# Kernel tuning notes

Measured on AMD Instinct MI355X. Metric: run time of the kernel, lower is better.

Reference implementation:

```python
import jax, jax.numpy as jnp
import numpy as np

C = 128          # num_channels
HID = 256        # mlp hidden = 2*C
HEAD_DIM = 16    # C // num_heads (8)
SCALE = 1.0 / np.sqrt(HEAD_DIM)
EPS = 1e-5


def _linear_init(key, fan_in, fan_out):
    kw, kb = jax.random.split(key)
    s = 1.0 / np.sqrt(fan_in)
    w = jax.random.uniform(kw, (fan_in, fan_out), minval=-s, maxval=s, dtype=jnp.float32)
    b = jax.random.uniform(kb, (fan_out,), minval=-s, maxval=s, dtype=jnp.float32)
    return w, b


def setup_inputs() -> dict:
    key = jax.random.key(0)
    ks = jax.random.split(key, 8)
    x = jax.random.normal(ks[0], (4, C, 64, 64), dtype=jnp.float32)
    wq, bq = _linear_init(ks[1], C, C)
    wk, bk = _linear_init(ks[2], C, C)
    wv, bv = _linear_init(ks[3], C, C)
    wo, bo = _linear_init(ks[4], C, C)
    w1, b1 = _linear_init(ks[5], C, HID)
    w2, b2 = _linear_init(ks[6], HID, C)
    return {
        "x": x,
        "ln1_w": jnp.ones((C,), jnp.float32), "ln1_b": jnp.zeros((C,), jnp.float32),
        "wq": wq, "bq": bq, "wk": wk, "bk": bk, "wv": wv, "bv": bv,
        "wo": wo, "bo": bo,
        "ln2_w": jnp.ones((C,), jnp.float32), "ln2_b": jnp.zeros((C,), jnp.float32),
        "w1": w1, "b1": b1, "w2": w2, "b2": b2,
    }


def _layernorm(x, w, b):
    mu = jnp.mean(x, axis=-1, keepdims=True)
    var = jnp.mean(jnp.square(x - mu), axis=-1, keepdims=True)
    return (x - mu) * jax.lax.rsqrt(var + EPS) * w + b


def reference(x, ln1_w, ln1_b, wq, bq, wk, bk, wv, bv, wo, bo, ln2_w, ln2_b, w1, b1, w2, b2):
    B, Cc, H, W = x.shape
    t = x.reshape(B, Cc, H * W).transpose(0, 2, 1)  # [B, S, C]
    xl = _layernorm(t, ln1_w, ln1_b)
    q = xl @ wq + bq
    k = xl @ wk + bk
    v = xl @ wv + bv
    scores = jnp.einsum('bqc,bkc->bqk', q, k) * SCALE  # [B, S, S]
    # Faithful to source: softmax over dim=1 (the QUERY axis).
    attn = jax.nn.softmax(scores, axis=1)
    att_out = jnp.einsum('bqk,bkc->bqc', attn, v) @ wo + bo
    t = att_out + t
    m = _layernorm(t, ln2_w, ln2_b) @ w1 + b1
    m = jax.nn.gelu(m, approximate=False) @ w2 + b2
    t = jax.nn.gelu(m, approximate=False) + t  # second GELU per source
    return t.transpose(0, 2, 1).reshape(B, Cc, H, W)
```

## Files before the change

kernel.cpp:

```cpp
#include <hip/hip_runtime.h>
#include <math.h>

#define S 4096
#define CNUM 128
#define BATCH 4
#define MTOT (BATCH * S)
#define SCLOG2E 0.36067376022224085f
#define EPSLN 1e-5f
#define KSPLIT 4
#define QSPLIT 8


typedef __attribute__((ext_vector_type(8))) short bf16x8;
typedef __attribute__((ext_vector_type(4))) float f32x4;
typedef __attribute__((ext_vector_type(16))) float f32x16;
typedef __attribute__((ext_vector_type(4))) unsigned int u32x4;

__device__ __forceinline__ float gelu_exact(float x) {
    return 0.5f * x * (1.0f + erff(x * 0.7071067811865476f));
}

__device__ __forceinline__ unsigned short f2b(float f) {
    union { float f; unsigned int u; } v; v.f = f;
    unsigned int r = (v.u + 0x7FFFu + ((v.u >> 16) & 1u)) >> 16;
    return (unsigned short)r;
}
__device__ __forceinline__ float b2f(unsigned short u) {
    return __uint_as_float((unsigned)u << 16);
}
__device__ __forceinline__ int swz(int col, int row) {
    return ((((col >> 3) ^ (row & 15)) << 3) | (col & 7));
}

__device__ __forceinline__ void gl_lds16(const void* g, void* l) {
    __builtin_amdgcn_global_load_lds(
        (__attribute__((address_space(1))) void*)g,
        (__attribute__((address_space(3))) void*)l, 16, 0, 0);
}

__global__ __launch_bounds__(256) void ln1_transpose(
    const float* __restrict__ x, const float* __restrict__ w, const float* __restrict__ bb,
    unsigned short* __restrict__ xlh, float* __restrict__ t)
{
    __shared__ float tile[128][65];
    __shared__ float mu[64], rs[64];
    const int b = blockIdx.y;
    const int s0 = blockIdx.x * 64;
    const float* xb = x + (size_t)b * CNUM * S;
    for (int i = threadIdx.x; i < 128 * 64; i += 256) {
        int c = i >> 6, sl = i & 63;
        tile[c][sl] = xb[(size_t)c * S + s0 + sl];
    }
    __syncthreads();
    if (threadIdx.x < 64) {
        float sum = 0.f, sq = 0.f;
        for (int c = 0; c < 128; ++c) {
            float v = tile[c][threadIdx.x];
            sum += v; sq += v * v;
        }
        float m = sum * (1.f / 128.f);
        float var = sq * (1.f / 128.f) - m * m;
        mu[threadIdx.x] = m;
        rs[threadIdx.x] = rsqrtf(var + EPSLN);
    }
    __syncthreads();
    for (int i = threadIdx.x; i < 128 * 64; i += 256) {
        int c = i & 127, sl = i >> 7;
        float v = tile[c][sl];
        size_t row = (size_t)b * S + s0 + sl;
        t[row * CNUM + c] = v;
        xlh[row * CNUM + swz(c, sl)] = f2b((v - mu[sl]) * rs[sl] * w[c] + bb[c]);
    }
}

__global__ __launch_bounds__(256) void convw(
    const float* __restrict__ wq, const float* __restrict__ wk, const float* __restrict__ wv,
    const float* __restrict__ wo, const float* __restrict__ w1, const float* __restrict__ w2,
    const float* __restrict__ bq, const float* __restrict__ bk, const float* __restrict__ bv,
    unsigned short* __restrict__ wqkvh, unsigned short* __restrict__ woh,
    unsigned short* __restrict__ w1h, unsigned short* __restrict__ w2h,
    float* __restrict__ bqkv)
{
    int a = blockIdx.y;
    int idx = blockIdx.x * 256 + threadIdx.x;
    if (a == 6) {
        if (idx < 128) bqkv[idx] = bq[idx];
        else if (idx < 256) bqkv[idx] = bk[idx - 128];
        else if (idx < 384) bqkv[idx] = bv[idx - 256];
        return;
    }
    const float* src; unsigned short* dst; int Nsh, Ksz;
    switch (a) {
        case 0: src = wq; dst = wqkvh;          Nsh = 7; Ksz = 128; break;
        case 1: src = wk; dst = wqkvh + 16384;  Nsh = 7; Ksz = 128; break;
        case 2: src = wv; dst = wqkvh + 32768;  Nsh = 7; Ksz = 128; break;
        case 3: src = wo; dst = woh;            Nsh = 7; Ksz = 128; break;
        case 4: src = w1; dst = w1h;            Nsh = 8; Ksz = 128; break;
        default: src = w2; dst = w2h;           Nsh = 7; Ksz = 256; break;
    }
    int total = Ksz << Nsh;
    if (idx >= total) return;
    int k = idx >> Nsh, n = idx & ((1 << Nsh) - 1);
    dst[n * Ksz + swz(k, n)] = f2b(src[idx]);
}

template<int KT, int EPI, int BM>
__global__ __launch_bounds__(256) void gemm_mfma(
    const unsigned short* __restrict__ A, const unsigned short* __restrict__ Bt,
    const float* __restrict__ bias, const float* __restrict__ res,
    void* __restrict__ Cv, void* __restrict__ Cv2,
    const float* __restrict__ wln, const float* __restrict__ bln, int N)
{
    constexpr int CH = KT / 8;
    constexpr int CSH = (KT == 128) ? 4 : 5;
    constexpr int BKT = (KT == 256) ? 128 : KT;
    constexpr int NPH = KT / BKT;
    constexpr int NJ = (BM == 64) ? 4 : 2;
    constexpr int NG = 128 / (NJ * 16);
    __shared__ unsigned short As[BM * KT];
    __shared__ unsigned short Bs[128 * BKT];
    __shared__ float2 lnred[(EPI == 3) ? NG * BM : 1];
    const int bm = blockIdx.y * BM;
    const int bn = blockIdx.x * 128;
    const int z = blockIdx.z;
    const unsigned short* Btz = (EPI == 7) ? Bt + z * 16384 : Bt;
    const float* biasz = (EPI == 7) ? bias + z * 128 : bias;
    const int tid = threadIdx.x;
    const int w = tid >> 6, l = tid & 63;
    const int rw = (BM == 64) ? (w & 1) * 32 : 0;
    const int cw = (BM == 64) ? (w >> 1) * 64 : w * 32;
    const int lm = l & 15, lq = l >> 4;

    f32x4 zero = {0.f, 0.f, 0.f, 0.f};
    f32x4 acc[2][NJ];
    #pragma unroll
    for (int i = 0; i < 2; ++i)
        #pragma unroll
        for (int j = 0; j < NJ; ++j) acc[i][j] = zero;

    #pragma unroll
    for (int ph = 0; ph < NPH; ++ph) {
        if (ph == 0) {
            if (EPI == 3) {
                #pragma unroll
                for (int i = 0; i < (BM * CH) / 256; ++i) {
                    int cid = i * 256 + tid;
                    int r = cid >> CSH, c = cid & (CH - 1);
                    int p = (c & ~15) | ((c ^ r) & 15);
                    float s8[8];
                    #pragma unroll
                    for (int j = 0; j < 8; ++j) s8[j] = 0.f;
                    #pragma unroll
                    for (int pp = 0; pp < KSPLIT; ++pp) {
                        const unsigned short* src = A + (size_t)pp * ((size_t)MTOT * CNUM)
                                                      + (size_t)(bm + r) * KT + c * 8;
                        ushort4 u0 = *(const ushort4*)(src);
                        ushort4 u1 = *(const ushort4*)(src + 4);
                        s8[0] += b2f(u0.x); s8[1] += b2f(u0.y); s8[2] += b2f(u0.z); s8[3] += b2f(u0.w);
                        s8[4] += b2f(u1.x); s8[5] += b2f(u1.y); s8[6] += b2f(u1.z); s8[7] += b2f(u1.w);
                    }
                    ushort4 o0, o1;
                    o0.x = f2b(s8[0]); o0.y = f2b(s8[1]); o0.z = f2b(s8[2]); o0.w = f2b(s8[3]);
                    o1.x = f2b(s8[4]); o1.y = f2b(s8[5]); o1.z = f2b(s8[6]); o1.w = f2b(s8[7]);
                    *(ushort4*)(As + r * KT + p * 8) = o0;
                    *(ushort4*)(As + r * KT + p * 8 + 4) = o1;
                }
            } else {
                #pragma unroll
                for (int i = 0; i < (BM * CH) / 256; ++i)
                    gl_lds16(A + (size_t)bm * KT + (i * 256 + tid) * 8,
                             As + (i * 256 + tid) * 8);
            }
        } else {
            __syncthreads();
        }
        #pragma unroll
        for (int i = 0; i < (128 * BKT / 8) / 256; ++i) {
            int cid = i * 256 + tid;
            int n = cid >> (CSH - (NPH - 1)), gg = cid & (BKT / 8 - 1);
            gl_lds16(Btz + (size_t)(bn + n) * KT + ph * BKT + gg * 8,
                     Bs + cid * 8);
        }
        __syncthreads();

        #pragma unroll
        for (int ks = 0; ks < BKT / 32; ++ks) {
            int c_loc = ks * 4 + lq;
            int c_glob = ph * 16 + c_loc;
            bf16x8 a[2], bfr[NJ];
            #pragma unroll
            for (int i = 0; i < 2; ++i) {
                int m = rw + i * 16 + lm;
                int p = (c_glob & ~15) | ((c_glob ^ m) & 15);
                a[i] = *(const bf16x8*)(As + m * KT + p * 8);
            }
            #pragma unroll
            for (int j = 0; j < NJ; ++j) {
                int n = cw + j * 16 + lm;
                int p = (c_loc ^ n) & 15;
                bfr[j] = *(const bf16x8*)(Bs + n * BKT + p * 8);
            }
            #pragma unroll
            for (int i = 0; i < 2; ++i)
                #pragma unroll
                for (int j = 0; j < NJ; ++j)
                    acc[i][j] = __builtin_amdgcn_mfma_f32_16x16x32_bf16(a[i], bfr[j], acc[i][j], 0, 0, 0);
        }
    }

    if (EPI == 3) {
        float vv[2][NJ][4];
        #pragma unroll
        for (int i = 0; i < 2; ++i) {
            int rowbase = bm + rw + i * 16 + lq * 4;
            #pragma unroll
            for (int j = 0; j < NJ; ++j) {
                int col = bn + cw + j * 16 + lm;
                #pragma unroll
                for (int reg = 0; reg < 4; ++reg)
                    vv[i][j][reg] = acc[i][j][reg] + biasz[col] +
                                    res[(size_t)(rowbase + reg) * N + col];
            }
        }
        #pragma unroll
        for (int i = 0; i < 2; ++i)
            #pragma unroll
            for (int reg = 0; reg < 4; ++reg) {
                float s = 0.f, q = 0.f;
                #pragma unroll
                for (int j = 0; j < NJ; ++j) {
                    float xv = vv[i][j][reg];
                    s += xv; q += xv * xv;
                }
                #pragma unroll
                for (int off = 1; off < 16; off <<= 1) {
                    s += __shfl_xor(s, off);
                    q += __shfl_xor(q, off);
                }
                if (lm == 0) {
                    float2 sq2; sq2.x = s; sq2.y = q;
                    lnred[(cw / (NJ * 16)) * BM + rw + i * 16 + lq * 4 + reg] = sq2;
                }
            }
        __syncthreads();
        #pragma unroll
        for (int i = 0; i < 2; ++i) {
            #pragma unroll
            for (int reg = 0; reg < 4; ++reg) {
                int lrow = rw + i * 16 + lq * 4 + reg;
                int row = bm + lrow;
                float sx = 0.f, sq = 0.f;
                #pragma unroll
                for (int g = 0; g < NG; ++g) {
                    float2 h = lnred[g * BM + lrow];
                    sx += h.x; sq += h.y;
                }
                float mean = sx * (1.f / 128.f);
                float var  = sq * (1.f / 128.f) - mean * mean;
                float rs = rsqrtf(var + EPSLN);
                #pragma unroll
                for (int j = 0; j < NJ; ++j) {
                    int col = bn + cw + j * 16 + lm;
                    float xv = vv[i][j][reg];
                    ((float*)Cv)[(size_t)row * N + col] = xv;
                    ((unsigned short*)Cv2)[(size_t)row * N + swz(col, lrow)] =
                        f2b((xv - mean) * rs * wln[col] + bln[col]);
                }
            }
        }
        return;
    }

    #pragma unroll
    for (int i = 0; i < 2; ++i) {
        int rowbase = bm + rw + i * 16 + lq * 4;
        #pragma unroll
        for (int j = 0; j < NJ; ++j) {
            int col = bn + cw + j * 16 + lm;
            float v[4];
            #pragma unroll
            for (int reg = 0; reg < 4; ++reg) v[reg] = acc[i][j][reg] + biasz[col];
            if (EPI == 6) {
                #pragma unroll
                for (int reg = 0; reg < 4; ++reg)
                    ((unsigned short*)Cv)[(size_t)(rowbase + reg) * N + swz(col, rowbase + reg)] =
                        f2b(gelu_exact(v[reg]));
            } else if (EPI == 8) {
                int bb = rowbase >> 12, s = rowbase & 4095;
                float4 o;
                o.x = gelu_exact(v[0]) + res[(size_t)(rowbase + 0) * N + col];
                o.y = gelu_exact(v[1]) + res[(size_t)(rowbase + 1) * N + col];
                o.z = gelu_exact(v[2]) + res[(size_t)(rowbase + 2) * N + col];
                o.w = gelu_exact(v[3]) + res[(size_t)(rowbase + 3) * N + col];
                *(float4*)(((float*)Cv) + ((size_t)(bb * 128 + col)) * 4096 + s) = o;
            } else if (EPI == 7) {
                if (z < 2) {
                    unsigned short* dst = ((unsigned short*)Cv) + (size_t)z * MTOT * 128;
                    #pragma unroll
                    for (int reg = 0; reg < 4; ++reg) {
                        float ov = (z == 0) ? v[reg] * SCLOG2E : v[reg];
                        dst[(size_t)(rowbase + reg) * 128 + swz(col, rowbase + reg)] = f2b(ov);
                    }
                } else {
                    int bb = rowbase >> 12, s = rowbase & 4095;
                    int kc = s >> 6, g = (s >> 3) & 7;
                    ushort4 o;
                    o.x = f2b(v[0]); o.y = f2b(v[1]); o.z = f2b(v[2]); o.w = f2b(v[3]);
                    *(ushort4*)(((unsigned short*)Cv) + (size_t)2 * MTOT * 128 +
                                (((size_t)bb * 64 + kc) << 13) +
                                col * 64 + ((g ^ (col & 7)) << 3) + (s & 7)) = o;
                }
            }
        }
    }
}

__global__ __launch_bounds__(256) void colsum(
    const unsigned short* __restrict__ qh, const unsigned short* __restrict__ kh,
    float* __restrict__ psum_all)
{
    __shared__ unsigned short Ks[128 * 128];
    __shared__ float csum[2][128];
    const int b = blockIdx.z;
    const unsigned short* Q = qh + (size_t)b * S * 128;
    const unsigned short* Km = kh + (size_t)b * S * 128;
    const int bn = blockIdx.x * 128;
    const int q0 = blockIdx.y * (S / QSPLIT);
    const int tid = threadIdx.x;
    const int w = tid >> 6, l = tid & 63;
    const int wr = (w >> 1) * 64, wc = (w & 1) * 64;
    const int lm = l & 15, lq = l >> 4;

    #pragma unroll
    for (int i = 0; i < 8; ++i)
        gl_lds16(Km + (size_t)bn * 128 + (i * 256 + tid) * 8, Ks + (i * 256 + tid) * 8);
    __syncthreads();

    float jsum[4] = {0.f, 0.f, 0.f, 0.f};
    for (int qt = 0; qt < (S / QSPLIT) / 128; ++qt) {
        f32x4 zero = {0.f, 0.f, 0.f, 0.f};
        f32x4 acc[4][4];
        #pragma unroll
        for (int i = 0; i < 4; ++i)
            #pragma unroll
            for (int j = 0; j < 4; ++j) acc[i][j] = zero;

        #pragma unroll
        for (int ks = 0; ks < 4; ++ks) {
            bf16x8 a[4], bfr[4];
            #pragma unroll
            for (int i = 0; i < 4; ++i) {
                int m = wr + i * 16 + lm;
                a[i] = *(const bf16x8*)(Q + (size_t)(q0 + qt * 128 + m) * 128 +
                                        (((ks * 4 + lq) ^ lm) << 3));
            }
            #pragma unroll
            for (int j = 0; j < 4; ++j) {
                int n = wc + j * 16 + lm;
                int p = (ks * 4 + lq) ^ (n & 15);
                bfr[j] = *(const bf16x8*)(Ks + n * 128 + p * 8);
            }
            #pragma unroll
            for (int i = 0; i < 4; ++i)
                #pragma unroll
                for (int j = 0; j < 4; ++j)
                    acc[i][j] = __builtin_amdgcn_mfma_f32_16x16x32_bf16(a[i], bfr[j], acc[i][j], 0, 0, 0);
        }

        #pragma unroll
        for (int i = 0; i < 4; ++i)
            #pragma unroll
            for (int j = 0; j < 4; ++j)
                #pragma unroll
                for (int reg = 0; reg < 4; ++reg)
                    jsum[j] += exp2f(acc[i][j][reg]);
    }

    #pragma unroll
    for (int j = 0; j < 4; ++j) {
        jsum[j] += __shfl_xor(jsum[j], 16);
        jsum[j] += __shfl_xor(jsum[j], 32);
    }
    if (l < 16) {
        #pragma unroll
        for (int j = 0; j < 4; ++j)
            csum[w >> 1][wc + j * 16 + l] = jsum[j];
    }
    __syncthreads();
    if (tid < 128)
        psum_all[((size_t)(blockIdx.y * BATCH + b)) * S + bn + tid] = csum[0][tid] + csum[1][tid];
}

__global__ __launch_bounds__(256) void vscale(
    unsigned short* __restrict__ Vimg_all, const float* __restrict__ psum_all)
{
    const int b = blockIdx.z;
    unsigned short* Vimg = Vimg_all + (size_t)b * CNUM * S;
    int i = (blockIdx.x * 256 + threadIdx.x) * 4;
    int kc = i >> 13;
    int off = i & 8191;
    int c = off >> 6;
    int p = (off >> 3) & 7;
    int g = p ^ (c & 7);
    int k = kc * 64 + g * 8 + (off & 7);
    float4 L = *(const float4*)(psum_all + (size_t)b * S + k);
    #pragma unroll
    for (int t = 1; t < QSPLIT; ++t) {
        float4 Lt = *(const float4*)(psum_all + ((size_t)(t * BATCH + b)) * S + k);
        L.x += Lt.x; L.y += Lt.y; L.z += Lt.z; L.w += Lt.w;
    }
    ushort4 v = *(ushort4*)(Vimg + i);
    v.x = f2b(b2f(v.x) / L.x);
    v.y = f2b(b2f(v.y) / L.y);
    v.z = f2b(b2f(v.z) / L.z);
    v.w = f2b(b2f(v.w) / L.w);
    *(ushort4*)(Vimg + i) = v;
}

__global__ __launch_bounds__(256, 2) void fused_attnv(
    const unsigned short* __restrict__ qh, const unsigned short* __restrict__ kh,
    const unsigned short* __restrict__ Vimg_all, unsigned short* __restrict__ parts)
{
    __shared__ unsigned short Ks[32 * 128];
    __shared__ unsigned short Vls[128 * 64];
    const int b = blockIdx.z;
    const unsigned short* Qm = qh + (size_t)b * S * 128;
    const unsigned short* Km = kh + (size_t)b * S * 128;
    const unsigned short* Vimg = Vimg_all + (((size_t)b * 64) << 13);
    unsigned short* Pout = parts + (size_t)blockIdx.x * ((size_t)MTOT * CNUM)
                                 + (size_t)b * S * CNUM;
    const int q0 = blockIdx.y * 128;
    const int kb0 = blockIdx.x * (S / KSPLIT);
    const int kc0 = blockIdx.x * (S / KSPLIT / 64);
    const int tid = threadIdx.x;
    const int w = tid >> 6, l = tid & 63;
    const int lc = l & 31, lh = l >> 5;
    const int row0 = q0 + w * 32;

    bf16x8 aq[8];
    #pragma unroll
    for (int d = 0; d < 8; ++d)
        aq[d] = *(const bf16x8*)(Qm + (size_t)(row0 + lc) * 128 +
                                 (((d * 2 + lh) ^ (lc & 15)) << 3));

    f32x16 acco[4];
    #pragma unroll
    for (int cb = 0; cb < 4; ++cb)
        #pragma unroll
        for (int r = 0; r < 16; ++r) acco[cb][r] = 0.f;

    for (int kt = 0; kt < S / KSPLIT / 32; ++kt) {
        const int kb = kb0 + kt * 32;
        if (kt) __syncthreads();
        #pragma unroll
        for (int i2 = 0; i2 < 2; ++i2)
            gl_lds16(Km + (size_t)kb * 128 + (i2 * 256 + tid) * 8,
                     Ks + (i2 * 256 + tid) * 8);
        if ((kt & 1) == 0) {
            const unsigned short* src = Vimg + ((size_t)(kc0 + (kt >> 1)) << 13) + tid * 8;
            #pragma unroll
            for (int i2 = 0; i2 < 4; ++i2)
                gl_lds16(src + i2 * 2048, &Vls[(i2 * 256 + tid) * 8]);
        }
        __syncthreads();

        f32x16 accT;
        #pragma unroll
        for (int r = 0; r < 16; ++r) accT[r] = 0.f;
        #pragma unroll
        for (int d = 0; d < 8; ++d) {
            int slot = d * 2 + lh;
            bf16x8 kf = *(const bf16x8*)(Ks + lc * 128 + ((slot ^ (lc & 15)) << 3));
            accT = __builtin_amdgcn_mfma_f32_32x32x16_bf16(kf, aq[d], accT, 0, 0, 0);
        }

        unsigned int pk[4][2];
        #pragma unroll
        for (int t = 0; t < 4; ++t)
            #pragma unroll
            for (int p = 0; p < 2; ++p) {
                float e0 = exp2f(accT[t * 4 + 2 * p]);
                float e1 = exp2f(accT[t * 4 + 2 * p + 1]);
                asm("v_cvt_pk_bf16_f32 %0, %1, %2" : "=v"(pk[t][p]) : "v"(e0), "v"(e1));
            }
        #pragma unroll
        for (int p = 0; p < 2; ++p) {
            asm volatile("v_permlane32_swap_b32 %0, %1" : "+v"(pk[0][p]), "+v"(pk[1][p]));
            asm volatile("v_permlane32_swap_b32 %0, %1" : "+v"(pk[2][p]), "+v"(pk[3][p]));
        }
        u32x4 u0 = {pk[0][0], pk[0][1], pk[1][0], pk[1][1]};
        u32x4 u1 = {pk[2][0], pk[2][1], pk[3][0], pk[3][1]};
        bf16x8 ap0 = __builtin_bit_cast(bf16x8, u0);
        bf16x8 ap1 = __builtin_bit_cast(bf16x8, u1);

        const int g0 = (kt & 1) * 4 + lh;
        const int g1 = g0 + 2;
        #pragma unroll
        for (int cb = 0; cb < 4; ++cb) {
            int c = cb * 32 + lc;
            bf16x8 v0 = *(const bf16x8*)(Vls + c * 64 + ((g0 ^ (c & 7)) << 3));
            bf16x8 v1 = *(const bf16x8*)(Vls + c * 64 + ((g1 ^ (c & 7)) << 3));
            acco[cb] = __builtin_amdgcn_mfma_f32_32x32x16_bf16(ap0, v0, acco[cb], 0, 0, 0);
            acco[cb] = __builtin_amdgcn_mfma_f32_32x32x16_bf16(ap1, v1, acco[cb], 0, 0, 0);
        }
    }

    #pragma unroll
    for (int cb = 0; cb < 4; ++cb)
        #pragma unroll
        for (int r = 0; r < 16; ++r) {
            int q = (r & 3) + 8 * (r >> 2) + 4 * lh;
            Pout[(size_t)(row0 + q) * CNUM + cb * 32 + lc] = f2b(acco[cb][r]);
        }
}

extern "C" void kernel_launch(void* const* d_in, const int* in_sizes, int n_in,
                              void* d_out, int out_size, void* d_ws, size_t ws_size,
                              hipStream_t stream)
{
    (void)in_sizes; (void)n_in; (void)out_size; (void)ws_size;
    const float* x    = (const float*)d_in[0];
    const float* ln1w = (const float*)d_in[1];
    const float* ln1b = (const float*)d_in[2];
    const float* wq   = (const float*)d_in[3];
    const float* bq   = (const float*)d_in[4];
    const float* wk   = (const float*)d_in[5];
    const float* bk   = (const float*)d_in[6];
    const float* wv   = (const float*)d_in[7];
    const float* bv   = (const float*)d_in[8];
    const float* wo   = (const float*)d_in[9];
    const float* bo   = (const float*)d_in[10];
    const float* ln2w = (const float*)d_in[11];
    const float* ln2b = (const float*)d_in[12];
    const float* w1   = (const float*)d_in[13];
    const float* b1   = (const float*)d_in[14];
    const float* w2   = (const float*)d_in[15];
    const float* b2   = (const float*)d_in[16];
    float* out = (float*)d_out;

    float* ws = (float*)d_ws;
    const size_t NSC = (size_t)MTOT * CNUM;
    float* t      = ws;
    float* y      = t + NSC;
    float* psum   = y + NSC;
    unsigned short* parts = (unsigned short*)(psum + (size_t)QSPLIT * BATCH * S);
    unsigned short* xlh = parts + (size_t)KSPLIT * NSC;
    unsigned short* qh  = xlh + NSC;
    unsigned short* kh  = qh + NSC;
    unsigned short* Vt  = kh + NSC;
    unsigned short* zh  = Vt + NSC;
    unsigned short* hh  = zh + NSC;
    unsigned short* wqkvh = hh + (size_t)MTOT * 256;
    unsigned short* woh = wqkvh + 3 * 16384;
    unsigned short* w1h = woh + 16384;
    unsigned short* w2h = w1h + 32768;
    float* bqkv = (float*)(w2h + 32768);

    ln1_transpose<<<dim3(S / 64, BATCH), 256, 0, stream>>>(x, ln1w, ln1b, xlh, t);
    convw<<<dim3(128, 7), 256, 0, stream>>>(wq, wk, wv, wo, w1, w2, bq, bk, bv,
                                            wqkvh, woh, w1h, w2h, bqkv);

    gemm_mfma<128, 7, 32><<<dim3(1, MTOT / 32, 3), 256, 0, stream>>>(
        xlh, wqkvh, bqkv, nullptr, qh, nullptr, nullptr, nullptr, 128);

    colsum<<<dim3(S / 128, QSPLIT, BATCH), 256, 0, stream>>>(qh, kh, psum);
    vscale<<<dim3(CNUM * S / 4 / 256, 1, BATCH), 256, 0, stream>>>(Vt, psum);
    fused_attnv<<<dim3(KSPLIT, S / 128, BATCH), 256, 0, stream>>>(qh, kh, Vt, parts);

    gemm_mfma<128, 3, 32><<<dim3(1, MTOT / 32), 256, 0, stream>>>(
        parts, woh, bo, t, y, zh, ln2w, ln2b, 128);
    gemm_mfma<128, 6, 32><<<dim3(2, MTOT / 32), 256, 0, stream>>>(
        zh, w1h, b1, nullptr, hh, nullptr, nullptr, nullptr, 256);
    gemm_mfma<256, 8, 32><<<dim3(1, MTOT / 32), 256, 0, stream>>>(
        hh, w2h, b2, y, out, nullptr, nullptr, nullptr, 128);
}
```

Before: 204.9 us.

## Fuse output projection, LayerNorm2 and MLP into one kernel

Replaces the three separate GEMM launches (Wo projection with residual and LN2, W1 with GELU, W2 with GELU and residual) with one kernel per 32-row tile. The LN output and hidden activations stay in shared memory instead of round-tripping through global buffers y, zh and hh. The generic gemm_mfma is reduced to the QKV path only. This removes intermediate global traffic and two launches. In exchange each block reloads every weight matrix serially and uses more LDS, which may limit occupancy and serialize weight loads with compute.

```diff
diff --git a/kernel.cpp b/kernel.cpp
--- a/kernel.cpp
+++ b/kernel.cpp
@@ -112,14 +112,9 @@
     const float* __restrict__ wln, const float* __restrict__ bln, int N)
 {
     constexpr int CH = KT / 8;
-    constexpr int CSH = (KT == 128) ? 4 : 5;
-    constexpr int BKT = (KT == 256) ? 128 : KT;
-    constexpr int NPH = KT / BKT;
     constexpr int NJ = (BM == 64) ? 4 : 2;
-    constexpr int NG = 128 / (NJ * 16);
     __shared__ unsigned short As[BM * KT];
-    __shared__ unsigned short Bs[128 * BKT];
-    __shared__ float2 lnred[(EPI == 3) ? NG * BM : 1];
+    __shared__ unsigned short Bs[128 * KT];
     const int bm = blockIdx.y * BM;
     const int bn = blockIdx.x * 128;
     const int z = blockIdx.z;
@@ -131,6 +126,14 @@
     const int cw = (BM == 64) ? (w >> 1) * 64 : w * 32;
     const int lm = l & 15, lq = l >> 4;
 
+    #pragma unroll
+    for (int i = 0; i < (BM * CH) / 256; ++i)
+        gl_lds16(A + (size_t)bm * KT + (i * 256 + tid) * 8, As + (i * 256 + tid) * 8);
+    #pragma unroll
+    for (int i = 0; i < (128 * CH) / 256; ++i)
+        gl_lds16(Btz + (size_t)bn * KT + (i * 256 + tid) * 8, Bs + (i * 256 + tid) * 8);
+    __syncthreads();
+
     f32x4 zero = {0.f, 0.f, 0.f, 0.f};
     f32x4 acc[2][NJ];
     #pragma unroll
@@ -139,136 +142,26 @@
         for (int j = 0; j < NJ; ++j) acc[i][j] = zero;
 
     #pragma unroll
-    for (int ph = 0; ph < NPH; ++ph) {
-        if (ph == 0) {
-            if (EPI == 3) {
-                #pragma unroll
-                for (int i = 0; i < (BM * CH) / 256; ++i) {
-                    int cid = i * 256 + tid;
-                    int r = cid >> CSH, c = cid & (CH - 1);
-                    int p = (c & ~15) | ((c ^ r) & 15);
-                    float s8[8];
-                    #pragma unroll
-                    for (int j = 0; j < 8; ++j) s8[j] = 0.f;
-                    #pragma unroll
-                    for (int pp = 0; pp < KSPLIT; ++pp) {
-                        const unsigned short* src = A + (size_t)pp * ((size_t)MTOT * CNUM)
-                                                      + (size_t)(bm + r) * KT + c * 8;
-                        ushort4 u0 = *(const ushort4*)(src);
-                        ushort4 u1 = *(const ushort4*)(src + 4);
-                        s8[0] += b2f(u0.x); s8[1] += b2f(u0.y); s8[2] += b2f(u0.z); s8[3] += b2f(u0.w);
-                        s8[4] += b2f(u1.x); s8[5] += b2f(u1.y); s8[6] += b2f(u1.z); s8[7] += b2f(u1.w);
-                    }
-                    ushort4 o0, o1;
-                    o0.x = f2b(s8[0]); o0.y = f2b(s8[1]); o0.z = f2b(s8[2]); o0.w = f2b(s8[3]);
-                    o1.x = f2b(s8[4]); o1.y = f2b(s8[5]); o1.z = f2b(s8[6]); o1.w = f2b(s8[7]);
-                    *(ushort4*)(As + r * KT + p * 8) = o0;
-                    *(ushort4*)(As + r * KT + p * 8 + 4) = o1;
-                }
-            } else {
-                #pragma unroll
-                for (int i = 0; i < (BM * CH) / 256; ++i)
-                    gl_lds16(A + (size_t)bm * KT + (i * 256 + tid) * 8,
-                             As + (i * 256 + tid) * 8);
-            }
-        } else {
-            __syncthreads();
-        }
-        #pragma unroll
-        for (int i = 0; i < (128 * BKT / 8) / 256; ++i) {
-            int cid = i * 256 + tid;
-            int n = cid >> (CSH - (NPH - 1)), gg = cid & (BKT / 8 - 1);
-            gl_lds16(Btz + (size_t)(bn + n) * KT + ph * BKT + gg * 8,
-                     Bs + cid * 8);
-        }
-        __syncthreads();
-
-        #pragma unroll
-        for (int ks = 0; ks < BKT / 32; ++ks) {
-            int c_loc = ks * 4 + lq;
-            int c_glob = ph * 16 + c_loc;
-            bf16x8 a[2], bfr[NJ];
-            #pragma unroll
-            for (int i = 0; i < 2; ++i) {
-                int m = rw + i * 16 + lm;
-                int p = (c_glob & ~15) | ((c_glob ^ m) & 15);
-                a[i] = *(const bf16x8*)(As + m * KT + p * 8);
-            }
-            #pragma unroll
-            for (int j = 0; j < NJ; ++j) {
-                int n = cw + j * 16 + lm;
-                int p = (c_loc ^ n) & 15;
-                bfr[j] = *(const bf16x8*)(Bs + n * BKT + p * 8);
-            }
-            #pragma unroll
-            for (int i = 0; i < 2; ++i)
-                #pragma unroll
-                for (int j = 0; j < NJ; ++j)
-                    acc[i][j] = __builtin_amdgcn_mfma_f32_16x16x32_bf16(a[i], bfr[j], acc[i][j], 0, 0, 0);
-        }
-    }
-
-    if (EPI == 3) {
-        float vv[2][NJ][4];
+    for (int ks = 0; ks < KT / 32; ++ks) {
+        int c_lin = ks * 4 + lq;
+        bf16x8 a[2], bfr[NJ];
         #pragma unroll
         for (int i = 0; i < 2; ++i) {
-            int rowbase = bm + rw + i * 16 + lq * 4;
-            #pragma unroll
-            for (int j = 0; j < NJ; ++j) {
-                int col = bn + cw + j * 16 + lm;
-                #pragma unroll
-                for (int reg = 0; reg < 4; ++reg)
-                    vv[i][j][reg] = acc[i][j][reg] + biasz[col] +
-                                    res[(size_t)(rowbase + reg) * N + col];
-            }
+            int m = rw + i * 16 + lm;
+            int p = (c_lin & ~15) | ((c_lin ^ m) & 15);
+            a[i] = *(const bf16x8*)(As + m * KT + p * 8);
+        }
+        #pragma unroll
+        for (int j = 0; j < NJ; ++j) {
+            int n = cw + j * 16 + lm;
+            int p = (c_lin & ~15) | ((c_lin ^ n) & 15);
+            bfr[j] = *(const bf16x8*)(Bs + n * KT + p * 8);
         }
         #pragma unroll
         for (int i = 0; i < 2; ++i)
             #pragma unroll
-            for (int reg = 0; reg < 4; ++reg) {
-                float s = 0.f, q = 0.f;
-                #pragma unroll
-                for (int j = 0; j < NJ; ++j) {
-                    float xv = vv[i][j][reg];
-                    s += xv; q += xv * xv;
-                }
-                #pragma unroll
-                for (int off = 1; off < 16; off <<= 1) {
-                    s += __shfl_xor(s, off);
-                    q += __shfl_xor(q, off);
-                }
-                if (lm == 0) {
-                    float2 sq2; sq2.x = s; sq2.y = q;
-                    lnred[(cw / (NJ * 16)) * BM + rw + i * 16 + lq * 4 + reg] = sq2;
-                }
-            }
-        __syncthreads();
-        #pragma unroll
-        for (int i = 0; i < 2; ++i) {
-            #pragma unroll
-            for (int reg = 0; reg < 4; ++reg) {
-                int lrow = rw + i * 16 + lq * 4 + reg;
-                int row = bm + lrow;
-                float sx = 0.f, sq = 0.f;
-                #pragma unroll
-                for (int g = 0; g < NG; ++g) {
-                    float2 h = lnred[g * BM + lrow];
-                    sx += h.x; sq += h.y;
-                }
-                float mean = sx * (1.f / 128.f);
-                float var  = sq * (1.f / 128.f) - mean * mean;
-                float rs = rsqrtf(var + EPSLN);
-                #pragma unroll
-                for (int j = 0; j < NJ; ++j) {
-                    int col = bn + cw + j * 16 + lm;
-                    float xv = vv[i][j][reg];
-                    ((float*)Cv)[(size_t)row * N + col] = xv;
-                    ((unsigned short*)Cv2)[(size_t)row * N + swz(col, lrow)] =
-                        f2b((xv - mean) * rs * wln[col] + bln[col]);
-                }
-            }
-        }
-        return;
+            for (int j = 0; j < NJ; ++j)
+                acc[i][j] = __builtin_amdgcn_mfma_f32_16x16x32_bf16(a[i], bfr[j], acc[i][j], 0, 0, 0);
     }
 
     #pragma unroll
@@ -280,36 +173,21 @@
             float v[4];
             #pragma unroll
             for (int reg = 0; reg < 4; ++reg) v[reg] = acc[i][j][reg] + biasz[col];
-            if (EPI == 6) {
+            if (z < 2) {
+                unsigned short* dst = ((unsigned short*)Cv) + (size_t)z * MTOT * 128;
                 #pragma unroll
-                for (int reg = 0; reg < 4; ++reg)
-                    ((unsigned short*)Cv)[(size_t)(rowbase + reg) * N + swz(col, rowbase + reg)] =
-                        f2b(gelu_exact(v[reg]));
-            } else if (EPI == 8) {
+                for (int reg = 0; reg < 4; ++reg) {
+                    float ov = (z == 0) ? v[reg] * SCLOG2E : v[reg];
+                    dst[(size_t)(rowbase + reg) * 128 + swz(col, rowbase + reg)] = f2b(ov);
+                }
+            } else {
                 int bb = rowbase >> 12, s = rowbase & 4095;
-                float4 o;
-                o.x = gelu_exact(v[0]) + res[(size_t)(rowbase + 0) * N + col];
-                o.y = gelu_exact(v[1]) + res[(size_t)(rowbase + 1) * N + col];
-                o.z = gelu_exact(v[2]) + res[(size_t)(rowbase + 2) * N + col];
-                o.w = gelu_exact(v[3]) + res[(size_t)(rowbase + 3) * N + col];
-                *(float4*)(((float*)Cv) + ((size_t)(bb * 128 + col)) * 4096 + s) = o;
-            } else if (EPI == 7) {
-                if (z < 2) {
-                    unsigned short* dst = ((unsigned short*)Cv) + (size_t)z * MTOT * 128;
-                    #pragma unroll
-                    for (int reg = 0; reg < 4; ++reg) {
-                        float ov = (z == 0) ? v[reg] * SCLOG2E : v[reg];
-                        dst[(size_t)(rowbase + reg) * 128 + swz(col, rowbase + reg)] = f2b(ov);
-                    }
-                } else {
-                    int bb = rowbase >> 12, s = rowbase & 4095;
-                    int kc = s >> 6, g = (s >> 3) & 7;
-                    ushort4 o;
-                    o.x = f2b(v[0]); o.y = f2b(v[1]); o.z = f2b(v[2]); o.w = f2b(v[3]);
-                    *(ushort4*)(((unsigned short*)Cv) + (size_t)2 * MTOT * 128 +
-                                (((size_t)bb * 64 + kc) << 13) +
-                                col * 64 + ((g ^ (col & 7)) << 3) + (s & 7)) = o;
-                }
+                int kc = s >> 6, g = (s >> 3) & 7;
+                ushort4 o;
+                o.x = f2b(v[0]); o.y = f2b(v[1]); o.z = f2b(v[2]); o.w = f2b(v[3]);
+                *(ushort4*)(((unsigned short*)Cv) + (size_t)2 * MTOT * 128 +
+                            (((size_t)bb * 64 + kc) << 13) +
+                            col * 64 + ((g ^ (col & 7)) << 3) + (s & 7)) = o;
             }
         }
     }
@@ -512,6 +390,239 @@
             int q = (r & 3) + 8 * (r >> 2) + 4 * lh;
             Pout[(size_t)(row0 + q) * CNUM + cb * 32 + lc] = f2b(acco[cb][r]);
         }
+}
+
+__global__ __launch_bounds__(256, 2) void mlp_fused(
+    const unsigned short* __restrict__ parts, const unsigned short* __restrict__ woh,
+    const unsigned short* __restrict__ w1h, const unsigned short* __restrict__ w2h,
+    const float* __restrict__ bo, const float* __restrict__ b1, const float* __restrict__ b2,
+    const float* __restrict__ tres, const float* __restrict__ wln, const float* __restrict__ bln,
+    float* __restrict__ out)
+{
+    __shared__ unsigned short As[32 * 128];
+    __shared__ unsigned short Bs[128 * 128];
+    __shared__ unsigned short zs[32 * 128];
+    __shared__ unsigned short hs[32 * 256];
+    __shared__ float2 lnred[4 * 32];
+    const int bm = blockIdx.x * 32;
+    const int tid = threadIdx.x;
+    const int w = tid >> 6, l = tid & 63;
+    const int cw = w * 32;
+    const int lm = l & 15, lq = l >> 4;
+    f32x4 zero = {0.f, 0.f, 0.f, 0.f};
+
+    #pragma unroll
+    for (int i = 0; i < 2; ++i) {
+        int cid = i * 256 + tid;
+        int r = cid >> 4, c = cid & 15;
+        int p = (c ^ r) & 15;
+        float s8[8];
+        #pragma unroll
+        for (int j = 0; j < 8; ++j) s8[j] = 0.f;
+        #pragma unroll
+        for (int pp = 0; pp < KSPLIT; ++pp) {
+            const unsigned short* src = parts + (size_t)pp * ((size_t)MTOT * CNUM)
+                                          + (size_t)(bm + r) * 128 + c * 8;
+            ushort4 u0 = *(const ushort4*)(src);
+            ushort4 u1 = *(const ushort4*)(src + 4);
+            s8[0] += b2f(u0.x); s8[1] += b2f(u0.y); s8[2] += b2f(u0.z); s8[3] += b2f(u0.w);
+            s8[4] += b2f(u1.x); s8[5] += b2f(u1.y); s8[6] += b2f(u1.z); s8[7] += b2f(u1.w);
+        }
+        ushort4 o0, o1;
+        o0.x = f2b(s8[0]); o0.y = f2b(s8[1]); o0.z = f2b(s8[2]); o0.w = f2b(s8[3]);
+        o1.x = f2b(s8[4]); o1.y = f2b(s8[5]); o1.z = f2b(s8[6]); o1.w = f2b(s8[7]);
+        *(ushort4*)(As + r * 128 + p * 8) = o0;
+        *(ushort4*)(As + r * 128 + p * 8 + 4) = o1;
+    }
+    #pragma unroll
+    for (int i = 0; i < 8; ++i)
+        gl_lds16(woh + (i * 256 + tid) * 8, Bs + (i * 256 + tid) * 8);
+    __syncthreads();
+
+    f32x4 acc[2][2];
+    #pragma unroll
+    for (int i = 0; i < 2; ++i) { acc[i][0] = zero; acc[i][1] = zero; }
+    #pragma unroll
+    for (int ks = 0; ks < 4; ++ks) {
+        int c = ks * 4 + lq;
+        bf16x8 a[2], bfr[2];
+        #pragma unroll
+        for (int i = 0; i < 2; ++i) {
+            int m = i * 16 + lm;
+            a[i] = *(const bf16x8*)(As + m * 128 + (((c ^ m) & 15) << 3));
+        }
+        #pragma unroll
+        for (int j = 0; j < 2; ++j) {
+            int n = cw + j * 16 + lm;
+            bfr[j] = *(const bf16x8*)(Bs + n * 128 + (((c ^ n) & 15) << 3));
+        }
+        #pragma unroll
+        for (int i = 0; i < 2; ++i)
+            #pragma unroll
+            for (int j = 0; j < 2; ++j)
+                acc[i][j] = __builtin_amdgcn_mfma_f32_16x16x32_bf16(a[i], bfr[j], acc[i][j], 0, 0, 0);
+    }
+    float vv[2][2][4];
+    #pragma unroll
+    for (int i = 0; i < 2; ++i) {
+        int rowbase = bm + i * 16 + lq * 4;
+        #pragma unroll
+        for (int j = 0; j < 2; ++j) {
+            int col = cw + j * 16 + lm;
+            #pragma unroll
+            for (int reg = 0; reg < 4; ++reg)
+                vv[i][j][reg] = acc[i][j][reg] + bo[col] +
+                                tres[(size_t)(rowbase + reg) * 128 + col];
+        }
+    }
+    #pragma unroll
+    for (int i = 0; i < 2; ++i)
+        #pragma unroll
+        for (int reg = 0; reg < 4; ++reg) {
+            float s = 0.f, q = 0.f;
+            #pragma unroll
+            for (int j = 0; j < 2; ++j) {
+                float xv = vv[i][j][reg];
+                s += xv; q += xv * xv;
+            }
+            #pragma unroll
+            for (int off = 1; off < 16; off <<= 1) {
+                s += __shfl_xor(s, off);
+                q += __shfl_xor(q, off);
+            }
+            if (lm == 0) {
+                float2 sq2; sq2.x = s; sq2.y = q;
+                lnred[w * 32 + i * 16 + lq * 4 + reg] = sq2;
+            }
+        }
+    __syncthreads();
+    #pragma unroll
+    for (int i = 0; i < 2; ++i) {
+        #pragma unroll
+        for (int reg = 0; reg < 4; ++reg) {
+            int lrow = i * 16 + lq * 4 + reg;
+            float sx = 0.f, sq = 0.f;
+            #pragma unroll
+            for (int g = 0; g < 4; ++g) {
+                float2 h = lnred[g * 32 + lrow];
+                sx += h.x; sq += h.y;
+            }
+            float mean = sx * (1.f / 128.f);
+            float var  = sq * (1.f / 128.f) - mean * mean;
+            float rs2 = rsqrtf(var + EPSLN);
+            #pragma unroll
+            for (int j = 0; j < 2; ++j) {
+                int col = cw + j * 16 + lm;
+                zs[lrow * 128 + swz(col, lrow)] =
+                    f2b((vv[i][j][reg] - mean) * rs2 * wln[col] + bln[col]);
+            }
+        }
+    }
+    #pragma unroll
+    for (int i = 0; i < 8; ++i)
+        gl_lds16(w1h + (i * 256 + tid) * 8, Bs + (i * 256 + tid) * 8);
+    __syncthreads();
+
+    #pragma unroll
+    for (int h = 0; h < 2; ++h) {
+        if (h) {
+            __syncthreads();
+            #pragma unroll
+            for (int i = 0; i < 8; ++i)
+                gl_lds16(w1h + 16384 + (i * 256 + tid) * 8, Bs + (i * 256 + tid) * 8);
+            __syncthreads();
+        }
+        f32x4 acc2[2][2];
+        #pragma unroll
+        for (int i = 0; i < 2; ++i) { acc2[i][0] = zero; acc2[i][1] = zero; }
+        #pragma unroll
+        for (int ks = 0; ks < 4; ++ks) {
+            int c = ks * 4 + lq;
+            bf16x8 a[2], bfr[2];
+            #pragma unroll
+            for (int i = 0; i < 2; ++i) {
+                int m = i * 16 + lm;
+                a[i] = *(const bf16x8*)(zs + m * 128 + (((c ^ m) & 15) << 3));
+            }
+            #pragma unroll
+            for (int j = 0; j < 2; ++j) {
+                int n = cw + j * 16 + lm;
+                bfr[j] = *(const bf16x8*)(Bs + n * 128 + (((c ^ n) & 15) << 3));
+            }
+            #pragma unroll
+            for (int i = 0; i < 2; ++i)
+                #pragma unroll
+                for (int j = 0; j < 2; ++j)
+                    acc2[i][j] = __builtin_amdgcn_mfma_f32_16x16x32_bf16(a[i], bfr[j], acc2[i][j], 0, 0, 0);
+        }
+        #pragma unroll
+        for (int i = 0; i < 2; ++i) {
+            #pragma unroll
+            for (int reg = 0; reg < 4; ++reg) {
+                int lrow = i * 16 + lq * 4 + reg;
+                #pragma unroll
+                for (int j = 0; j < 2; ++j) {
+                    int col = h * 128 + cw + j * 16 + lm;
+                    hs[lrow * 256 + swz(col, lrow)] =
+                        f2b(gelu_exact(acc2[i][j][reg] + b1[col]));
+                }
+            }
+        }
+    }
+    __syncthreads();
+
+    f32x4 acc3[2][2];
+    #pragma unroll
+    for (int i = 0; i < 2; ++i) { acc3[i][0] = zero; acc3[i][1] = zero; }
+    #pragma unroll
+    for (int ph = 0; ph < 2; ++ph) {
+        #pragma unroll
+        for (int i = 0; i < 8; ++i) {
+            int cid = i * 256 + tid;
+            int n = cid >> 4, gg = cid & 15;
+            gl_lds16(w2h + (size_t)n * 256 + ph * 128 + gg * 8, Bs + cid * 8);
+        }
+        __syncthreads();
+        #pragma unroll
+        for (int ks = 0; ks < 4; ++ks) {
+            int c_loc = ks * 4 + lq;
+            int c_glob = ph * 16 + c_loc;
+            bf16x8 a[2], bfr[2];
+            #pragma unroll
+            for (int i = 0; i < 2; ++i) {
+                int m = i * 16 + lm;
+                int p = (c_glob & ~15) | ((c_glob ^ m) & 15);
+                a[i] = *(const bf16x8*)(hs + m * 256 + p * 8);
+            }
+            #pragma unroll
+            for (int j = 0; j < 2; ++j) {
+                int n = cw + j * 16 + lm;
+                bfr[j] = *(const bf16x8*)(Bs + n * 128 + (((c_loc ^ n) & 15) << 3));
+            }
+            #pragma unroll
+            for (int i = 0; i < 2; ++i)
+                #pragma unroll
+                for (int j = 0; j < 2; ++j)
+                    acc3[i][j] = __builtin_amdgcn_mfma_f32_16x16x32_bf16(a[i], bfr[j], acc3[i][j], 0, 0, 0);
+        }
+        if (ph == 0) __syncthreads();
+    }
+
+    #pragma unroll
+    for (int i = 0; i < 2; ++i) {
+        int rowbase = bm + i * 16 + lq * 4;
+        int bb = rowbase >> 12, s = rowbase & 4095;
+        #pragma unroll
+        for (int j = 0; j < 2; ++j) {
+            int col = cw + j * 16 + lm;
+            float4 o;
+            o.x = gelu_exact(acc3[i][j][0] + b2[col]) + vv[i][j][0];
+            o.y = gelu_exact(acc3[i][j][1] + b2[col]) + vv[i][j][1];
+            o.z = gelu_exact(acc3[i][j][2] + b2[col]) + vv[i][j][2];
+            o.w = gelu_exact(acc3[i][j][3] + b2[col]) + vv[i][j][3];
+            *(float4*)(out + ((size_t)(bb * 128 + col)) * 4096 + s) = o;
+        }
+    }
 }
 
 extern "C" void kernel_launch(void* const* d_in, const int* in_sizes, int n_in,
@@ -544,7 +655,7 @@
     float* y      = t + NSC;
     float* psum   = y + NSC;
     unsigned short* parts = (unsigned short*)(psum + (size_t)QSPLIT * BATCH * S);
-    unsigned short* xlh = parts + (size_t)KSPLIT * NSC;
+    unsigned short* xlh = parts + (size_t)8 * NSC;
     unsigned short* qh  = xlh + NSC;
     unsigned short* kh  = qh + NSC;
     unsigned short* Vt  = kh + NSC;
@@ -567,10 +678,6 @@
     vscale<<<dim3(CNUM * S / 4 / 256, 1, BATCH), 256, 0, stream>>>(Vt, psum);
     fused_attnv<<<dim3(KSPLIT, S / 128, BATCH), 256, 0, stream>>>(qh, kh, Vt, parts);
 
-    gemm_mfma<128, 3, 32><<<dim3(1, MTOT / 32), 256, 0, stream>>>(
-        parts, woh, bo, t, y, zh, ln2w, ln2b, 128);
-    gemm_mfma<128, 6, 32><<<dim3(2, MTOT / 32), 256, 0, stream>>>(
-        zh, w1h, b1, nullptr, hh, nullptr, nullptr, nullptr, 256);
-    gemm_mfma<256, 8, 32><<<dim3(1, MTOT / 32), 256, 0, stream>>>(
-        hh, w2h, b2, y, out, nullptr, nullptr, nullptr, 128);
-}
+    mlp_fused<<<MTOT / 32, 256, 0, stream>>>(
+        parts, woh, w1h, w2h, bo, b1, b2, t, ln2w, ln2b, out);
+}
```

Result: faster. 199.8 us (-2.5%).
